# Kernel tuning notes

Measured on AMD Instinct MI355X. Metric: run time of the kernel, lower is better.

## Reference

```python
import jax, jax.numpy as jnp
import numpy as np

N, E, NFEAT, NHID = 50000, 800000, 256, 128
EPS = 1e-5


def setup_inputs() -> dict:
    key = jax.random.key(0)
    ks = jax.random.split(key, 12)
    s = 0.05
    return {
        "x": jax.random.normal(ks[0], (N, NFEAT), jnp.float32),
        "adj": jax.random.randint(ks[1], (2, E), 0, N, jnp.int32),
        "features": jax.random.uniform(ks[2], (E,), jnp.float32),
        "W_in": jax.random.normal(ks[3], (NHID, NFEAT), jnp.float32) * s,
        "b_in": jnp.zeros((NHID,), jnp.float32),
        "W1_rel": jax.random.normal(ks[4], (NHID, NHID), jnp.float32) * s,
        "b1_rel": jnp.zeros((NHID,), jnp.float32),
        "W1_root": jax.random.normal(ks[5], (NHID, NHID), jnp.float32) * s,
        "W2_rel": jax.random.normal(ks[6], (NHID, NHID), jnp.float32) * s,
        "b2_rel": jnp.zeros((NHID,), jnp.float32),
        "W2_root": jax.random.normal(ks[7], (NHID, NHID), jnp.float32) * s,
        "gamma": jnp.ones((NHID,), jnp.float32),
        "beta": jnp.zeros((NHID,), jnp.float32),
    }


def _graph_conv(h, src, dst, ew, W_rel, b_rel, W_root):
    # torch_geometric GraphConv (aggr='add'):
    #   out_i = W_rel @ (sum_{j->i} e_ji * h_j) + b_rel + W_root @ h_i
    msg = h[src] * ew[:, None]                       # [E, NHID] gather
    agg = jax.ops.segment_sum(msg, dst, num_segments=N)  # [N, NHID] scatter-add
    return agg @ W_rel.T + b_rel + h @ W_root.T


def _batch_norm(h, gamma, beta):
    mu = h.mean(axis=0)
    var = h.var(axis=0)
    return (h - mu) * jax.lax.rsqrt(var + EPS) * gamma + beta


def reference(x, adj, features, W_in, b_in, W1_rel, b1_rel, W1_root,
              W2_rel, b2_rel, W2_root, gamma, beta):
    src, dst = adj[0], adj[1]
    h = jax.nn.relu(x @ W_in.T + b_in)               # linear_in + relu (dropout=identity in eval)
    h = _graph_conv(h, src, dst, features, W1_rel, b1_rel, W1_root)
    h = jax.nn.relu(_batch_norm(h, gamma, beta))     # batch1 + relu
    h = _graph_conv(h, src, dst, features, W2_rel, b2_rel, W2_root)
    return _batch_norm(h, gamma, beta)               # batch1 reused (per source)
```

## Files before the change

### kernel.cpp

```cpp
#include <hip/hip_runtime.h>
#include <hip/hip_bf16.h>

#define NNODES 50000
#define NEDGES 800000
#define NF 256
#define NH 128
#define BN_EPS 1e-5f
#define MTILES (NNODES / 16)
#define GEMM_BLOCKS 512
#define NBUCKETS 196
#define BCAP 4608
#define SCAT_BLOCKS ((NEDGES + 2047) / 2048)

typedef __attribute__((ext_vector_type(8))) __bf16 bf16x8;
typedef __attribute__((ext_vector_type(4))) float floatx4;

__device__ __forceinline__ __hip_bfloat16 f2bf(float f) { return __float2bfloat16(f); }
__device__ __forceinline__ float bits2f(unsigned short b) {
    union { unsigned u; float f; } u; u.u = ((unsigned)b) << 16; return u.f;
}

__device__ __forceinline__ bf16x8 cvt8(const float* __restrict__ p) {
    floatx4 a0 = *(const floatx4*)p;
    floatx4 a1 = *(const floatx4*)(p + 4);
    bf16x8 r;
    r[0] = (__bf16)a0[0]; r[1] = (__bf16)a0[1]; r[2] = (__bf16)a0[2]; r[3] = (__bf16)a0[3];
    r[4] = (__bf16)a1[0]; r[5] = (__bf16)a1[1]; r[6] = (__bf16)a1[2]; r[7] = (__bf16)a1[3];
    return r;
}

__global__ __launch_bounds__(256) void convert_w_kernel(
    const float* __restrict__ W_in, const float* __restrict__ W1r,
    const float* __restrict__ W1o, const float* __restrict__ W2r,
    const float* __restrict__ W2o, __hip_bfloat16* __restrict__ wbf,
    int* __restrict__ gcursor)
{
    const int i = blockIdx.x * 256 + threadIdx.x;
    if (blockIdx.x == 0 && threadIdx.x < NBUCKETS)
        gcursor[threadIdx.x] = threadIdx.x * BCAP;
    const float* src; int off;
    if (i < 32768)      { src = W_in; off = i; }
    else if (i < 49152) { src = W1r;  off = i - 32768; }
    else if (i < 65536) { src = W1o;  off = i - 49152; }
    else if (i < 81920) { src = W2r;  off = i - 65536; }
    else                { src = W2o;  off = i - 81920; }
    wbf[i] = f2bf(src[off]);
}

__global__ __launch_bounds__(256) void bucket_scatter_kernel(
    const int* __restrict__ adj, const float* __restrict__ ew,
    int* __restrict__ gcursor, uint2* __restrict__ pairbuf,
    unsigned char* __restrict__ nodebuf)
{
    __shared__ int cnt[NBUCKETS];
    __shared__ int base[NBUCKETS];
    const int tid = threadIdx.x;
    if (tid < NBUCKETS) cnt[tid] = 0;
    __syncthreads();
    const int e0 = blockIdx.x * 2048;
    #pragma unroll
    for (int i = 0; i < 8; ++i) {
        const int e = e0 + i * 256 + tid;
        if (e < NEDGES) atomicAdd(&cnt[adj[NEDGES + e] >> 8], 1);
    }
    __syncthreads();
    if (tid < NBUCKETS) {
        base[tid] = atomicAdd(&gcursor[tid], cnt[tid]);
        cnt[tid] = 0;
    }
    __syncthreads();
    #pragma unroll
    for (int i = 0; i < 8; ++i) {
        const int e = e0 + i * 256 + tid;
        if (e >= NEDGES) continue;
        const int dst = adj[NEDGES + e];
        const int b = dst >> 8;
        const int off = atomicAdd(&cnt[b], 1);
        const int slot = base[b] + off;
        if (slot < (b + 1) * BCAP) {
            pairbuf[slot] = make_uint2((unsigned)adj[e], __float_as_uint(ew[e]));
            nodebuf[slot] = (unsigned char)(dst & 255);
        }
    }
}

__global__ __launch_bounds__(256) void bucket_sort_kernel(
    const int* __restrict__ gcursor, const uint2* __restrict__ pairbuf,
    const unsigned char* __restrict__ nodebuf, uint2* __restrict__ sorted,
    int* __restrict__ rowptr, int* __restrict__ rowend)
{
    const int b = blockIdx.x;
    const int tid = threadIdx.x;
    const int capbase = b * BCAP;
    int n = gcursor[b] - capbase;
    if (n > BCAP) n = BCAP;

    __shared__ int cnt[256];
    __shared__ int s[256];
    cnt[tid] = 0;
    __syncthreads();
    for (int j = tid; j < n; j += 256)
        atomicAdd(&cnt[nodebuf[capbase + j]], 1);
    __syncthreads();
    const int v = cnt[tid];
    s[tid] = v;
    __syncthreads();
    for (int off = 1; off < 256; off <<= 1) {
        const int t = (tid >= off) ? s[tid - off] : 0;
        __syncthreads();
        s[tid] += t;
        __syncthreads();
    }
    const int excl = s[tid] - v;
    const int node = b * 256 + tid;
    if (node < NNODES) {
        rowptr[node] = capbase + excl;
        rowend[node] = capbase + excl + v;
    }
    cnt[tid] = excl;
    __syncthreads();
    for (int j = tid; j < n; j += 256) {
        const int nd = nodebuf[capbase + j];
        const int pos = atomicAdd(&cnt[nd], 1);
        sorted[capbase + pos] = pairbuf[capbase + j];
    }
}

__global__ __launch_bounds__(256, 2) void gemm_in_kernel(
    const float* __restrict__ X, const __hip_bfloat16* __restrict__ W,
    const float* __restrict__ bias, __hip_bfloat16* __restrict__ out)
{
    const int waveG = blockIdx.x * 4 + (threadIdx.x >> 6);
    const int lane = threadIdx.x & 63;
    const int half = waveG & 1;
    const int ar = lane & 15;
    const int q  = lane >> 4;

    bf16x8 bw[4][8];
    float bv[4];
    #pragma unroll
    for (int t = 0; t < 4; ++t) {
        const int row = half * 64 + t * 16 + ar;
        bv[t] = bias[row];
        #pragma unroll
        for (int k = 0; k < 8; ++k)
            bw[t][k] = *(const bf16x8*)(W + (size_t)row * NF + k * 32 + q * 8);
    }

    for (int strip = waveG >> 1; strip < MTILES; strip += GEMM_BLOCKS * 2) {
        const int m0 = strip << 4;
        floatx4 acc[4] = {};
        #pragma unroll
        for (int k = 0; k < 8; ++k) {
            const bf16x8 a = cvt8(X + (size_t)(m0 + ar) * NF + k * 32 + q * 8);
            #pragma unroll
            for (int t = 0; t < 4; ++t)
                acc[t] = __builtin_amdgcn_mfma_f32_16x16x32_bf16(a, bw[t][k], acc[t], 0, 0, 0);
        }
        #pragma unroll
        for (int t = 0; t < 4; ++t) {
            const int col = half * 64 + t * 16 + ar;
            #pragma unroll
            for (int r = 0; r < 4; ++r) {
                const float v = fmaxf(acc[t][r] + bv[t], 0.f);
                out[(size_t)(m0 + q * 4 + r) * NH + col] = f2bf(v);
            }
        }
    }
}

__global__ __launch_bounds__(256) void gather_kernel(
    const uint2* __restrict__ sorted, const int* __restrict__ rowptr,
    const int* __restrict__ rowend,
    const __hip_bfloat16* __restrict__ h, __hip_bfloat16* __restrict__ agg)
{
    const int node = blockIdx.x * 4 + (threadIdx.x >> 6);
    if (node >= NNODES) return;
    const int lane = threadIdx.x & 63;
    const int beg = rowptr[node];
    const int end = rowend[node];
    const unsigned short* hb = (const unsigned short*)h;

    float p0 = 0.f, p1 = 0.f, q0 = 0.f, q1 = 0.f;
    float r0 = 0.f, r1 = 0.f, s0 = 0.f, s1 = 0.f;

    int j = beg;
    if ((j & 1) && j < end) {
        const uint2 ev = sorted[j++];
        const float w = __uint_as_float(ev.y);
        const unsigned raw = *(const unsigned*)(hb + (size_t)ev.x * NH + lane * 2);
        p0 += w * bits2f((unsigned short)(raw & 0xffffu));
        p1 += w * bits2f((unsigned short)(raw >> 16));
    }
    for (; j + 4 <= end; j += 4) {
        const uint4 e01 = *(const uint4*)(sorted + j);
        const uint4 e23 = *(const uint4*)(sorted + j + 2);
        const unsigned ra = *(const unsigned*)(hb + (size_t)e01.x * NH + lane * 2);
        const unsigned rb = *(const unsigned*)(hb + (size_t)e01.z * NH + lane * 2);
        const unsigned rc = *(const unsigned*)(hb + (size_t)e23.x * NH + lane * 2);
        const unsigned rd = *(const unsigned*)(hb + (size_t)e23.z * NH + lane * 2);
        const float wa = __uint_as_float(e01.y), wb = __uint_as_float(e01.w);
        const float wc = __uint_as_float(e23.y), wd = __uint_as_float(e23.w);
        p0 += wa * bits2f((unsigned short)(ra & 0xffffu));
        p1 += wa * bits2f((unsigned short)(ra >> 16));
        q0 += wb * bits2f((unsigned short)(rb & 0xffffu));
        q1 += wb * bits2f((unsigned short)(rb >> 16));
        r0 += wc * bits2f((unsigned short)(rc & 0xffffu));
        r1 += wc * bits2f((unsigned short)(rc >> 16));
        s0 += wd * bits2f((unsigned short)(rd & 0xffffu));
        s1 += wd * bits2f((unsigned short)(rd >> 16));
    }
    for (; j < end; ++j) {
        const uint2 ev = sorted[j];
        const float w = __uint_as_float(ev.y);
        const unsigned raw = *(const unsigned*)(hb + (size_t)ev.x * NH + lane * 2);
        p0 += w * bits2f((unsigned short)(raw & 0xffffu));
        p1 += w * bits2f((unsigned short)(raw >> 16));
    }
    const float a0 = (p0 + q0) + (r0 + s0);
    const float a1 = (p1 + q1) + (r1 + s1);
    unsigned o = ((unsigned)__bfloat16_as_ushort(f2bf(a1)) << 16) |
                 (unsigned)__bfloat16_as_ushort(f2bf(a0));
    *(unsigned*)((unsigned short*)agg + (size_t)node * NH + lane * 2) = o;
}

__global__ __launch_bounds__(256, 2) void gemm_conv_kernel(
    const __hip_bfloat16* __restrict__ agg, const __hip_bfloat16* __restrict__ h,
    const __hip_bfloat16* __restrict__ Wrel, const __hip_bfloat16* __restrict__ Wroot,
    const float* __restrict__ bias, float* __restrict__ out,
    float* __restrict__ partial)
{
    const int waveG = blockIdx.x * 4 + (threadIdx.x >> 6);
    const int lane = threadIdx.x & 63;
    const int half = waveG & 1;
    const int ar = lane & 15;
    const int q  = lane >> 4;

    bf16x8 brel[4][4], brt[4][4];
    float bv[4];
    #pragma unroll
    for (int t = 0; t < 4; ++t) {
        const int row = half * 64 + t * 16 + ar;
        bv[t] = bias[row];
        #pragma unroll
        for (int k = 0; k < 4; ++k) {
            brel[t][k] = *(const bf16x8*)(Wrel + (size_t)row * NH + k * 32 + q * 8);
            brt[t][k]  = *(const bf16x8*)(Wroot + (size_t)row * NH + k * 32 + q * 8);
        }
    }

    float s1[4] = {}, s2[4] = {};

    for (int strip = waveG >> 1; strip < MTILES; strip += GEMM_BLOCKS * 2) {
        const int m0 = strip << 4;
        floatx4 acc[4] = {};
        #pragma unroll
        for (int k = 0; k < 4; ++k) {
            const bf16x8 a = *(const bf16x8*)(agg + (size_t)(m0 + ar) * NH + k * 32 + q * 8);
            #pragma unroll
            for (int t = 0; t < 4; ++t)
                acc[t] = __builtin_amdgcn_mfma_f32_16x16x32_bf16(a, brel[t][k], acc[t], 0, 0, 0);
        }
        #pragma unroll
        for (int k = 0; k < 4; ++k) {
            const bf16x8 a = *(const bf16x8*)(h + (size_t)(m0 + ar) * NH + k * 32 + q * 8);
            #pragma unroll
            for (int t = 0; t < 4; ++t)
                acc[t] = __builtin_amdgcn_mfma_f32_16x16x32_bf16(a, brt[t][k], acc[t], 0, 0, 0);
        }
        #pragma unroll
        for (int t = 0; t < 4; ++t) {
            const int col = half * 64 + t * 16 + ar;
            #pragma unroll
            for (int r = 0; r < 4; ++r) {
                const float v = acc[t][r] + bv[t];
                out[(size_t)(m0 + q * 4 + r) * NH + col] = v;
                s1[t] += v; s2[t] += v * v;
            }
        }
    }

    __shared__ float sst[256];
    sst[threadIdx.x] = 0.f;
    __syncthreads();
    #pragma unroll
    for (int t = 0; t < 4; ++t) {
        float a = s1[t], b = s2[t];
        a += __shfl_xor(a, 16, 64); a += __shfl_xor(a, 32, 64);
        b += __shfl_xor(b, 16, 64); b += __shfl_xor(b, 32, 64);
        if (q == 0) {
            const int col = half * 64 + t * 16 + ar;
            atomicAdd(&sst[col], a);
            atomicAdd(&sst[128 + col], b);
        }
    }
    __syncthreads();
    partial[blockIdx.x * 256 + threadIdx.x] = sst[threadIdx.x];
}

__global__ __launch_bounds__(256) void reduce_stats_kernel(
    const float* __restrict__ partial, float* __restrict__ stats)
{
    const int tid = threadIdx.x;
    float a = 0.f, b = 0.f, c = 0.f, d = 0.f;
    for (int blk = 0; blk < GEMM_BLOCKS; blk += 4) {
        a += partial[(blk + 0) * 256 + tid];
        b += partial[(blk + 1) * 256 + tid];
        c += partial[(blk + 2) * 256 + tid];
        d += partial[(blk + 3) * 256 + tid];
    }
    stats[tid] = (a + b) + (c + d);
}

__global__ __launch_bounds__(256) void bn_relu_bf16_kernel(
    const float* __restrict__ t, const float* __restrict__ stats,
    const float* __restrict__ gamma, const float* __restrict__ beta,
    __hip_bfloat16* __restrict__ out)
{
    const size_t i = (size_t)blockIdx.x * blockDim.x + threadIdx.x;
    const int c = (int)(i & (NH - 1));
    const float inv_n = 1.0f / (float)NNODES;
    const float mu = stats[c] * inv_n;
    const float var = stats[128 + c] * inv_n - mu * mu;
    const float rs = rsqrtf(var + BN_EPS);
    float v = (t[i] - mu) * rs * gamma[c] + beta[c];
    out[i] = f2bf(fmaxf(v, 0.f));
}

__global__ __launch_bounds__(256) void bn_f32_kernel(
    const float* __restrict__ t, const float* __restrict__ stats,
    const float* __restrict__ gamma, const float* __restrict__ beta,
    float* __restrict__ out)
{
    const size_t i = (size_t)blockIdx.x * blockDim.x + threadIdx.x;
    const int c = (int)(i & (NH - 1));
    const float inv_n = 1.0f / (float)NNODES;
    const float mu = stats[c] * inv_n;
    const float var = stats[128 + c] * inv_n - mu * mu;
    const float rs = rsqrtf(var + BN_EPS);
    out[i] = (t[i] - mu) * rs * gamma[c] + beta[c];
}


extern "C" void kernel_launch(void* const* d_in, const int* in_sizes, int n_in,
                              void* d_out, int out_size, void* d_ws, size_t ws_size,
                              hipStream_t stream)
{
    const float* x    = (const float*)d_in[0];
    const int*   adj  = (const int*)d_in[1];
    const float* ew   = (const float*)d_in[2];
    const float* W_in = (const float*)d_in[3];
    const float* b_in = (const float*)d_in[4];
    const float* W1r  = (const float*)d_in[5];
    const float* b1   = (const float*)d_in[6];
    const float* W1o  = (const float*)d_in[7];
    const float* W2r  = (const float*)d_in[8];
    const float* b2   = (const float*)d_in[9];
    const float* W2o  = (const float*)d_in[10];
    const float* gmm  = (const float*)d_in[11];
    const float* bta  = (const float*)d_in[12];
    float* out = (float*)d_out;
    float* t   = (float*)d_out;

    char* ws = (char*)d_ws;
    __hip_bfloat16* h0  = (__hip_bfloat16*)ws; ws += (size_t)NNODES * NH * 2;
    __hip_bfloat16* h1  = (__hip_bfloat16*)ws; ws += (size_t)NNODES * NH * 2;
    __hip_bfloat16* agg = (__hip_bfloat16*)ws; ws += (size_t)NNODES * NH * 2;
    uint2*          sorted  = (uint2*)ws;      ws += (size_t)NBUCKETS * BCAP * 8;
    uint2*          pairbuf = (uint2*)ws;      ws += (size_t)NBUCKETS * BCAP * 8;
    unsigned char*  nodebuf = (unsigned char*)ws; ws += (size_t)NBUCKETS * BCAP;
    int*            rowptr  = (int*)ws;        ws += NNODES * 4;
    int*            rowend  = (int*)ws;        ws += NNODES * 4;
    int*            gcursor = (int*)ws;        ws += ((NBUCKETS + 3) & ~3) * 4;
    __hip_bfloat16* wbf     = (__hip_bfloat16*)ws; ws += 98304 * 2;
    float*          partial = (float*)ws;      ws += GEMM_BLOCKS * 256 * 4;
    float*          st      = (float*)ws;      ws += 256 * 4;

    const __hip_bfloat16* Wb_in = wbf;
    const __hip_bfloat16* Wb1r  = wbf + 32768;
    const __hip_bfloat16* Wb1o  = wbf + 49152;
    const __hip_bfloat16* Wb2r  = wbf + 65536;
    const __hip_bfloat16* Wb2o  = wbf + 81920;

    const int node_blocks = (NNODES + 3) / 4;
    const int bn_blocks   = (NNODES * NH) / 256;

    convert_w_kernel<<<98304 / 256, 256, 0, stream>>>(W_in, W1r, W1o, W2r, W2o, wbf, gcursor);
    bucket_scatter_kernel<<<SCAT_BLOCKS, 256, 0, stream>>>(adj, ew, gcursor, pairbuf, nodebuf);
    bucket_sort_kernel<<<NBUCKETS, 256, 0, stream>>>(gcursor, pairbuf, nodebuf,
                                                     sorted, rowptr, rowend);

    gemm_in_kernel<<<GEMM_BLOCKS, 256, 0, stream>>>(x, Wb_in, b_in, h0);
    gather_kernel<<<node_blocks, 256, 0, stream>>>(sorted, rowptr, rowend, h0, agg);
    gemm_conv_kernel<<<GEMM_BLOCKS, 256, 0, stream>>>(agg, h0, Wb1r, Wb1o, b1, t, partial);
    reduce_stats_kernel<<<1, 256, 0, stream>>>(partial, st);
    bn_relu_bf16_kernel<<<bn_blocks, 256, 0, stream>>>(t, st, gmm, bta, h1);

    gather_kernel<<<node_blocks, 256, 0, stream>>>(sorted, rowptr, rowend, h1, agg);
    gemm_conv_kernel<<<GEMM_BLOCKS, 256, 0, stream>>>(agg, h1, Wb2r, Wb2o, b2, t, partial);
    reduce_stats_kernel<<<1, 256, 0, stream>>>(partial, st);
    bn_f32_kernel<<<bn_blocks, 256, 0, stream>>>(t, st, gmm, bta, out);
}
```

Measured before the change: 337.3 us.

## Fuse edge gather into graph-conv GEMM via shared-memory aggregate tiles

Merges the separate gather and conv-GEMM kernels into one gconv kernel. Each block builds a 16-node aggregate tile in LDS, with each wave gathering a 32-feature slice per node using 16-byte loads, then runs MFMA on it directly. This removes the write and re-read of the bf16 agg buffer and one launch per layer. In exchange, only 16 lanes per wave walk edges, each through its own node's list, so divergence follows the maximum degree in the tile. Each block also hits two barriers per tile.

```diff
diff --git a/kernel.cpp b/kernel.cpp
--- a/kernel.cpp
+++ b/kernel.cpp
@@ -8,6 +8,7 @@
 #define BN_EPS 1e-5f
 #define MTILES (NNODES / 16)
 #define GEMM_BLOCKS 512
+#define GCONV_BLOCKS 512
 #define NBUCKETS 196
 #define BCAP 4608
 #define SCAT_BLOCKS ((NEDGES + 2047) / 2048)
@@ -16,9 +17,6 @@
 typedef __attribute__((ext_vector_type(4))) float floatx4;
 
 __device__ __forceinline__ __hip_bfloat16 f2bf(float f) { return __float2bfloat16(f); }
-__device__ __forceinline__ float bits2f(unsigned short b) {
-    union { unsigned u; float f; } u; u.u = ((unsigned)b) << 16; return u.f;
-}
 
 __device__ __forceinline__ bf16x8 cvt8(const float* __restrict__ p) {
     floatx4 a0 = *(const floatx4*)p;
@@ -169,127 +167,94 @@
     }
 }
 
-__global__ __launch_bounds__(256) void gather_kernel(
+__global__ __launch_bounds__(256, 3) void gconv_kernel(
     const uint2* __restrict__ sorted, const int* __restrict__ rowptr,
-    const int* __restrict__ rowend,
-    const __hip_bfloat16* __restrict__ h, __hip_bfloat16* __restrict__ agg)
-{
-    const int node = blockIdx.x * 4 + (threadIdx.x >> 6);
-    if (node >= NNODES) return;
-    const int lane = threadIdx.x & 63;
-    const int beg = rowptr[node];
-    const int end = rowend[node];
-    const unsigned short* hb = (const unsigned short*)h;
-
-    float p0 = 0.f, p1 = 0.f, q0 = 0.f, q1 = 0.f;
-    float r0 = 0.f, r1 = 0.f, s0 = 0.f, s1 = 0.f;
-
-    int j = beg;
-    if ((j & 1) && j < end) {
-        const uint2 ev = sorted[j++];
-        const float w = __uint_as_float(ev.y);
-        const unsigned raw = *(const unsigned*)(hb + (size_t)ev.x * NH + lane * 2);
-        p0 += w * bits2f((unsigned short)(raw & 0xffffu));
-        p1 += w * bits2f((unsigned short)(raw >> 16));
-    }
-    for (; j + 4 <= end; j += 4) {
-        const uint4 e01 = *(const uint4*)(sorted + j);
-        const uint4 e23 = *(const uint4*)(sorted + j + 2);
-        const unsigned ra = *(const unsigned*)(hb + (size_t)e01.x * NH + lane * 2);
-        const unsigned rb = *(const unsigned*)(hb + (size_t)e01.z * NH + lane * 2);
-        const unsigned rc = *(const unsigned*)(hb + (size_t)e23.x * NH + lane * 2);
-        const unsigned rd = *(const unsigned*)(hb + (size_t)e23.z * NH + lane * 2);
-        const float wa = __uint_as_float(e01.y), wb = __uint_as_float(e01.w);
-        const float wc = __uint_as_float(e23.y), wd = __uint_as_float(e23.w);
-        p0 += wa * bits2f((unsigned short)(ra & 0xffffu));
-        p1 += wa * bits2f((unsigned short)(ra >> 16));
-        q0 += wb * bits2f((unsigned short)(rb & 0xffffu));
-        q1 += wb * bits2f((unsigned short)(rb >> 16));
-        r0 += wc * bits2f((unsigned short)(rc & 0xffffu));
-        r1 += wc * bits2f((unsigned short)(rc >> 16));
-        s0 += wd * bits2f((unsigned short)(rd & 0xffffu));
-        s1 += wd * bits2f((unsigned short)(rd >> 16));
-    }
-    for (; j < end; ++j) {
-        const uint2 ev = sorted[j];
-        const float w = __uint_as_float(ev.y);
-        const unsigned raw = *(const unsigned*)(hb + (size_t)ev.x * NH + lane * 2);
-        p0 += w * bits2f((unsigned short)(raw & 0xffffu));
-        p1 += w * bits2f((unsigned short)(raw >> 16));
-    }
-    const float a0 = (p0 + q0) + (r0 + s0);
-    const float a1 = (p1 + q1) + (r1 + s1);
-    unsigned o = ((unsigned)__bfloat16_as_ushort(f2bf(a1)) << 16) |
-                 (unsigned)__bfloat16_as_ushort(f2bf(a0));
-    *(unsigned*)((unsigned short*)agg + (size_t)node * NH + lane * 2) = o;
-}
-
-__global__ __launch_bounds__(256, 2) void gemm_conv_kernel(
-    const __hip_bfloat16* __restrict__ agg, const __hip_bfloat16* __restrict__ h,
+    const int* __restrict__ rowend, const __hip_bfloat16* __restrict__ h,
     const __hip_bfloat16* __restrict__ Wrel, const __hip_bfloat16* __restrict__ Wroot,
     const float* __restrict__ bias, float* __restrict__ out,
     float* __restrict__ partial)
 {
-    const int waveG = blockIdx.x * 4 + (threadIdx.x >> 6);
+    const int u    = threadIdx.x >> 6;
     const int lane = threadIdx.x & 63;
-    const int half = waveG & 1;
-    const int ar = lane & 15;
-    const int q  = lane >> 4;
-
-    bf16x8 brel[4][4], brt[4][4];
-    float bv[4];
-    #pragma unroll
-    for (int t = 0; t < 4; ++t) {
-        const int row = half * 64 + t * 16 + ar;
-        bv[t] = bias[row];
+    const int ar   = lane & 15;
+    const int q    = lane >> 4;
+
+    bf16x8 brel[2][4], brt[2][4];
+    float bv[2];
+    #pragma unroll
+    for (int tt = 0; tt < 2; ++tt) {
+        const int row = (2 * u + tt) * 16 + ar;
+        bv[tt] = bias[row];
         #pragma unroll
         for (int k = 0; k < 4; ++k) {
-            brel[t][k] = *(const bf16x8*)(Wrel + (size_t)row * NH + k * 32 + q * 8);
-            brt[t][k]  = *(const bf16x8*)(Wroot + (size_t)row * NH + k * 32 + q * 8);
-        }
-    }
-
-    float s1[4] = {}, s2[4] = {};
-
-    for (int strip = waveG >> 1; strip < MTILES; strip += GEMM_BLOCKS * 2) {
-        const int m0 = strip << 4;
-        floatx4 acc[4] = {};
+            brel[tt][k] = *(const bf16x8*)(Wrel + (size_t)row * NH + k * 32 + q * 8);
+            brt[tt][k]  = *(const bf16x8*)(Wroot + (size_t)row * NH + k * 32 + q * 8);
+        }
+    }
+
+    __shared__ __hip_bfloat16 fragbuf[4 * 512];
+    __shared__ float sst[256];
+
+    float s1[2] = {}, s2[2] = {};
+    const int feat_off = u * 32 + q * 8;
+
+    for (int s = blockIdx.x; s < MTILES; s += GCONV_BLOCKS) {
+        const int m0 = s << 4;
+        const int node = m0 + ar;
+
+        int cur = rowptr[node];
+        const int end = rowend[node];
+        float ga[8] = {};
+        while (__any(cur < end)) {
+            if (cur < end) {
+                const uint2 ev = sorted[cur++];
+                const float w = __uint_as_float(ev.y);
+                const bf16x8 c = *(const bf16x8*)(h + (size_t)ev.x * NH + feat_off);
+                #pragma unroll
+                for (int i = 0; i < 8; ++i) ga[i] += w * (float)c[i];
+            }
+        }
+        bf16x8 myfrag;
+        #pragma unroll
+        for (int i = 0; i < 8; ++i) myfrag[i] = (__bf16)ga[i];
+        *(bf16x8*)(fragbuf + u * 512 + lane * 8) = myfrag;
+        __syncthreads();
+
+        floatx4 acc[2] = {};
         #pragma unroll
         for (int k = 0; k < 4; ++k) {
-            const bf16x8 a = *(const bf16x8*)(agg + (size_t)(m0 + ar) * NH + k * 32 + q * 8);
-            #pragma unroll
-            for (int t = 0; t < 4; ++t)
-                acc[t] = __builtin_amdgcn_mfma_f32_16x16x32_bf16(a, brel[t][k], acc[t], 0, 0, 0);
+            const bf16x8 a = *(const bf16x8*)(fragbuf + k * 512 + lane * 8);
+            acc[0] = __builtin_amdgcn_mfma_f32_16x16x32_bf16(a, brel[0][k], acc[0], 0, 0, 0);
+            acc[1] = __builtin_amdgcn_mfma_f32_16x16x32_bf16(a, brel[1][k], acc[1], 0, 0, 0);
         }
         #pragma unroll
         for (int k = 0; k < 4; ++k) {
             const bf16x8 a = *(const bf16x8*)(h + (size_t)(m0 + ar) * NH + k * 32 + q * 8);
-            #pragma unroll
-            for (int t = 0; t < 4; ++t)
-                acc[t] = __builtin_amdgcn_mfma_f32_16x16x32_bf16(a, brt[t][k], acc[t], 0, 0, 0);
-        }
-        #pragma unroll
-        for (int t = 0; t < 4; ++t) {
-            const int col = half * 64 + t * 16 + ar;
+            acc[0] = __builtin_amdgcn_mfma_f32_16x16x32_bf16(a, brt[0][k], acc[0], 0, 0, 0);
+            acc[1] = __builtin_amdgcn_mfma_f32_16x16x32_bf16(a, brt[1][k], acc[1], 0, 0, 0);
+        }
+        #pragma unroll
+        for (int tt = 0; tt < 2; ++tt) {
+            const int col = (2 * u + tt) * 16 + ar;
             #pragma unroll
             for (int r = 0; r < 4; ++r) {
-                const float v = acc[t][r] + bv[t];
+                const float v = acc[tt][r] + bv[tt];
                 out[(size_t)(m0 + q * 4 + r) * NH + col] = v;
-                s1[t] += v; s2[t] += v * v;
+                s1[tt] += v; s2[tt] += v * v;
             }
         }
-    }
-
-    __shared__ float sst[256];
+        __syncthreads();
+    }
+
     sst[threadIdx.x] = 0.f;
     __syncthreads();
     #pragma unroll
-    for (int t = 0; t < 4; ++t) {
-        float a = s1[t], b = s2[t];
+    for (int tt = 0; tt < 2; ++tt) {
+        float a = s1[tt], b = s2[tt];
         a += __shfl_xor(a, 16, 64); a += __shfl_xor(a, 32, 64);
         b += __shfl_xor(b, 16, 64); b += __shfl_xor(b, 32, 64);
         if (q == 0) {
-            const int col = half * 64 + t * 16 + ar;
+            const int col = (2 * u + tt) * 16 + ar;
             atomicAdd(&sst[col], a);
             atomicAdd(&sst[128 + col], b);
         }
@@ -303,7 +268,7 @@
 {
     const int tid = threadIdx.x;
     float a = 0.f, b = 0.f, c = 0.f, d = 0.f;
-    for (int blk = 0; blk < GEMM_BLOCKS; blk += 4) {
+    for (int blk = 0; blk < GCONV_BLOCKS; blk += 4) {
         a += partial[(blk + 0) * 256 + tid];
         b += partial[(blk + 1) * 256 + tid];
         c += partial[(blk + 2) * 256 + tid];
@@ -365,7 +330,6 @@
     char* ws = (char*)d_ws;
     __hip_bfloat16* h0  = (__hip_bfloat16*)ws; ws += (size_t)NNODES * NH * 2;
     __hip_bfloat16* h1  = (__hip_bfloat16*)ws; ws += (size_t)NNODES * NH * 2;
-    __hip_bfloat16* agg = (__hip_bfloat16*)ws; ws += (size_t)NNODES * NH * 2;
     uint2*          sorted  = (uint2*)ws;      ws += (size_t)NBUCKETS * BCAP * 8;
     uint2*          pairbuf = (uint2*)ws;      ws += (size_t)NBUCKETS * BCAP * 8;
     unsigned char*  nodebuf = (unsigned char*)ws; ws += (size_t)NBUCKETS * BCAP;
@@ -373,7 +337,7 @@
     int*            rowend  = (int*)ws;        ws += NNODES * 4;
     int*            gcursor = (int*)ws;        ws += ((NBUCKETS + 3) & ~3) * 4;
     __hip_bfloat16* wbf     = (__hip_bfloat16*)ws; ws += 98304 * 2;
-    float*          partial = (float*)ws;      ws += GEMM_BLOCKS * 256 * 4;
+    float*          partial = (float*)ws;      ws += GCONV_BLOCKS * 256 * 4;
     float*          st      = (float*)ws;      ws += 256 * 4;
 
     const __hip_bfloat16* Wb_in = wbf;
@@ -382,8 +346,7 @@
     const __hip_bfloat16* Wb2r  = wbf + 65536;
     const __hip_bfloat16* Wb2o  = wbf + 81920;
 
-    const int node_blocks = (NNODES + 3) / 4;
-    const int bn_blocks   = (NNODES * NH) / 256;
+    const int bn_blocks = (NNODES * NH) / 256;
 
     convert_w_kernel<<<98304 / 256, 256, 0, stream>>>(W_in, W1r, W1o, W2r, W2o, wbf, gcursor);
     bucket_scatter_kernel<<<SCAT_BLOCKS, 256, 0, stream>>>(adj, ew, gcursor, pairbuf, nodebuf);
@@ -391,13 +354,13 @@
                                                      sorted, rowptr, rowend);
 
     gemm_in_kernel<<<GEMM_BLOCKS, 256, 0, stream>>>(x, Wb_in, b_in, h0);
-    gather_kernel<<<node_blocks, 256, 0, stream>>>(sorted, rowptr, rowend, h0, agg);
-    gemm_conv_kernel<<<GEMM_BLOCKS, 256, 0, stream>>>(agg, h0, Wb1r, Wb1o, b1, t, partial);
+    gconv_kernel<<<GCONV_BLOCKS, 256, 0, stream>>>(sorted, rowptr, rowend, h0,
+                                                   Wb1r, Wb1o, b1, t, partial);
     reduce_stats_kernel<<<1, 256, 0, stream>>>(partial, st);
     bn_relu_bf16_kernel<<<bn_blocks, 256, 0, stream>>>(t, st, gmm, bta, h1);
 
-    gather_kernel<<<node_blocks, 256, 0, stream>>>(sorted, rowptr, rowend, h1, agg);
-    gemm_conv_kernel<<<GEMM_BLOCKS, 256, 0, stream>>>(agg, h1, Wb2r, Wb2o, b2, t, partial);
+    gconv_kernel<<<GCONV_BLOCKS, 256, 0, stream>>>(sorted, rowptr, rowend, h1,
+                                                   Wb2r, Wb2o, b2, t, partial);
     reduce_stats_kernel<<<1, 256, 0, stream>>>(partial, st);
     bn_f32_kernel<<<bn_blocks, 256, 0, stream>>>(t, st, gmm, bta, out);
 }
```

Result: slower. 470.8 us (+39.6%).
